# Kernel optimization log

Measured on AMD Instinct MI355X. Metric: run time of the kernel, lower is better.

Reference implementation:

```python
import jax, jax.numpy as jnp
import numpy as np

BS, LS, LL = 8, 64, 256          # batch, target len, source len
PS, D, NL, NH = 16000, 512, 4, 8 # vocab, d_model, n_layer, n_heads
DH = D // NH
DF = 4 * D


def _layer_norm(x, g, b, eps=1e-5):
    m = jnp.mean(x, -1, keepdims=True)
    v = jnp.var(x, -1, keepdims=True)
    return (x - m) * jax.lax.rsqrt(v + eps) * g + b


def setup_inputs() -> dict:
    key = jax.random.key(0)
    ks = jax.random.split(key, 20)
    s = 0.02
    return {
        "attn": jax.random.uniform(ks[0], (BS, LS, LL), jnp.float32),
        "mask": jnp.ones((BS, LL), dtype=bool),
        "tgt": jax.random.randint(ks[1], (BS, LS), 0, PS),
        "emb_w": jax.random.normal(ks[2], (PS, D), jnp.float32) * s,
        "Wq": jax.random.normal(ks[3], (NL, D, D), jnp.float32) * s,
        "Wk": jax.random.normal(ks[4], (NL, D, D), jnp.float32) * s,
        "Wv": jax.random.normal(ks[5], (NL, D, D), jnp.float32) * s,
        "Wo": jax.random.normal(ks[6], (NL, D, D), jnp.float32) * s,
        "ln1_g": jnp.ones((NL, D), jnp.float32),
        "ln1_b": jnp.zeros((NL, D), jnp.float32),
        "W1": jax.random.normal(ks[7], (NL, D, DF), jnp.float32) * s,
        "b1": jnp.zeros((NL, DF), jnp.float32),
        "W2": jax.random.normal(ks[8], (NL, DF, D), jnp.float32) * s,
        "b2": jnp.zeros((NL, D), jnp.float32),
        "ln2_g": jnp.ones((NL, D), jnp.float32),
        "ln2_b": jnp.zeros((NL, D), jnp.float32),
        "proj_w": jax.random.normal(ks[9], (PS, D), jnp.float32) * s,
    }


def reference(attn, mask, tgt, emb_w, Wq, Wk, Wv, Wo, ln1_g, ln1_b,
              W1, b1, W2, b2, ln2_g, ln2_b, proj_w):
    bs, ls = tgt.shape
    ll = attn.shape[2]
    ps = emb_w.shape[0]

    # --- scatter-add attention rows into vocab-aligned matrix (index_put_ accumulate=True) ---
    idx = (jnp.arange(bs)[:, None] * ps + tgt).reshape(-1)          # (bs*ls,)
    alg = jax.ops.segment_sum(attn.reshape(-1, ll), idx,
                              num_segments=bs * ps)                 # (bs*ps, ll)
    alg = alg.reshape(bs, ps, ll).transpose(0, 2, 1)                # (bs, ll, ps)
    alg = alg.at[:, :, 0].set(0.0)                                  # index_fill_ vocab id 0

    # --- transformer encoder over source positions ---
    x = alg @ emb_w                                                 # (bs, ll, D)
    pos = jnp.arange(ll, dtype=jnp.float32)[:, None]
    div = jnp.exp(jnp.arange(0, D, 2, dtype=jnp.float32) * (-np.log(10000.0) / D))
    pe = jnp.zeros((ll, D), jnp.float32)
    pe = pe.at[:, 0::2].set(jnp.sin(pos * div)).at[:, 1::2].set(jnp.cos(pos * div))
    x = x * np.sqrt(D).astype(np.float32) + pe

    bias = jnp.where(mask[:, None, None, :], 0.0, -1e9).astype(x.dtype)  # (bs,1,1,ll)
    scale = 1.0 / np.sqrt(DH).astype(np.float32)
    for i in range(Wq.shape[0]):
        q = (x @ Wq[i]).reshape(bs, ll, NH, DH)
        k = (x @ Wk[i]).reshape(bs, ll, NH, DH)
        v = (x @ Wv[i]).reshape(bs, ll, NH, DH)
        s = jnp.einsum('bqhd,bkhd->bhqk', q, k) * scale + bias
        a = jax.nn.softmax(s, axis=-1)
        o = jnp.einsum('bhqk,bkhd->bqhd', a, v).reshape(bs, ll, D) @ Wo[i]
        x = _layer_norm(x + o, ln1_g[i], ln1_b[i])
        f = jax.nn.relu(x @ W1[i] + b1[i]) @ W2[i] + b2[i]
        x = _layer_norm(x + f, ln2_g[i], ln2_b[i])

    return x @ proj_w.T                                             # (bs, ll, ps)
```

## Files before the change

kernel.cpp:

```cpp
#include <hip/hip_runtime.h>
#include <hip/hip_bf16.h>

#define BS 8
#define LS 64
#define LL 256
#define PS 16000
#define D  512
#define NL 4
#define NH 8
#define DH 64
#define DF 2048
#define ROWS (BS*LL)

typedef __attribute__((ext_vector_type(8))) __bf16 bf16x8;
typedef __attribute__((ext_vector_type(4))) float f32x4;
typedef __hip_bfloat16 hbf16;

static __device__ inline unsigned short f2bfu(float f) {
  hbf16 h = __float2bfloat16(f);
  return *reinterpret_cast<unsigned short*>(&h);
}

#define GLL16(g, l) __builtin_amdgcn_global_load_lds( \
    (const __attribute__((address_space(1))) unsigned int*)(g), \
    (__attribute__((address_space(3))) unsigned int*)(l), 16, 0, 0)

__global__ __launch_bounds__(256) void init_kernel(
    const float* __restrict__ Wq, const float* __restrict__ Wk,
    const float* __restrict__ Wv, const float* __restrict__ Wo,
    const float* __restrict__ W1, const float* __restrict__ W2,
    const float* __restrict__ proj,
    const float* __restrict__ attn, const int* __restrict__ tgt,
    const float* __restrict__ emb,
    hbf16* __restrict__ qkvT, hbf16* __restrict__ woT,
    hbf16* __restrict__ w1T, hbf16* __restrict__ w2T,
    hbf16* __restrict__ projT, hbf16* __restrict__ xb) {
  int id = blockIdx.x;
  if (id >= 14288) {
    int bl = id - 14288;
    int b = bl >> 8, l = bl & 255;
    int d0 = threadIdx.x;
    const float* ap = attn + (size_t)(b*LS)*LL + l;
    const int* tp = tgt + b*LS;
    float acc0 = 0.f, acc1 = 0.f;
    for (int s = 0; s < LS; ++s) {
      int t = tp[s];
      if (t != 0) {
        float a = ap[s*LL];
        acc0 = fmaf(a, emb[(size_t)t*D + d0],        acc0);
        acc1 = fmaf(a, emb[(size_t)t*D + d0 + 256],  acc1);
      }
    }
    const float sq = 22.62741699796952f;
    const float c  = -9.210340371976184f / 512.0f;
    {
      int d = d0;
      float freq = expf((float)(2*(d >> 1)) * c);
      float ang = (float)l * freq;
      float pe = (d & 1) ? cosf(ang) : sinf(ang);
      xb[(size_t)bl*D + d] = __float2bfloat16(acc0 * sq + pe);
    }
    {
      int d = d0 + 256;
      float freq = expf((float)(2*(d >> 1)) * c);
      float ang = (float)l * freq;
      float pe = (d & 1) ? cosf(ang) : sinf(ang);
      xb[(size_t)bl*D + d] = __float2bfloat16(acc1 * sq + pe);
    }
    return;
  }
  if (id >= 12288) {
    int i = (id - 12288) * 4096 + threadIdx.x * 4;
#pragma unroll
    for (int q = 0; q < 4; ++q) {
      int j = i + q*1024;
      float4 w = *(const float4*)(proj + j);
      ushort4 o;
      o.x = f2bfu(w.x); o.y = f2bfu(w.y); o.z = f2bfu(w.z); o.w = f2bfu(w.w);
      *(ushort4*)(projT + j) = o;
    }
    return;
  }
  const float* src; hbf16* dst; int R, C, r0, c0;
  if (id < 3072) {
    int zz = id >> 8, t = id & 255;
    int layer = zz / 3, which = zz % 3;
    src = (which == 0 ? Wq : which == 1 ? Wk : Wv) + (size_t)layer*D*D;
    dst = qkvT + (size_t)layer*3*D*D + (size_t)which*D*D;
    R = D; C = D; r0 = (t >> 4)*32; c0 = (t & 15)*32;
  } else if (id < 4096) {
    int t = id - 3072; int zz = t >> 8; t &= 255;
    src = Wo + (size_t)zz*D*D; dst = woT + (size_t)zz*D*D;
    R = D; C = D; r0 = (t >> 4)*32; c0 = (t & 15)*32;
  } else if (id < 8192) {
    int t = id - 4096; int zz = t >> 10; t &= 1023;
    src = W1 + (size_t)zz*D*DF; dst = w1T + (size_t)zz*D*DF;
    R = D; C = DF; r0 = (t >> 6)*32; c0 = (t & 63)*32;
  } else {
    int t = id - 8192; int zz = t >> 10; t &= 1023;
    src = W2 + (size_t)zz*DF*D; dst = w2T + (size_t)zz*DF*D;
    R = DF; C = D; r0 = (t >> 4)*32; c0 = (t & 15)*32;
  }
  __shared__ float tls[32][33];
  int tx = threadIdx.x & 31, ty = threadIdx.x >> 5;
#pragma unroll
  for (int i = 0; i < 4; ++i)
    tls[ty + i*8][tx] = src[(size_t)(r0 + ty + i*8)*C + c0 + tx];
  __syncthreads();
#pragma unroll
  for (int i = 0; i < 4; ++i)
    dst[(size_t)(c0 + ty + i*8)*R + r0 + tx] = __float2bfloat16(tls[tx][ty + i*8]);
}

template<int MF, int OUTMODE, int HASBIAS, int RELU, int BMODE, int SWZ>
__global__ __launch_bounds__(512) void mgemm(
    const __bf16* __restrict__ A, const __bf16* __restrict__ B,
    const float* __restrict__ bias, void* __restrict__ C0,
    __bf16* __restrict__ vt, int N, int K, int lda, int ldb, int ldc) {
  constexpr int TM = MF * 64;
  constexpr int NA = MF / 2;
  __shared__ __bf16 As[3][TM*32];
  __shared__ __bf16 Bs[3][128*32];
  const int z = blockIdx.z;
  if (BMODE == 3) {
    A += (size_t)z*K;
    B += (size_t)z*K;
    C0 = (void*)((char*)C0 + (size_t)z*ROWS*ldc*(OUTMODE == 0 ? 4 : 2));
  }
  int bm, bn;
  if (SWZ) {
    int nwg = gridDim.x * gridDim.y;
    int flat = blockIdx.y * gridDim.x + blockIdx.x;
    int swz = (flat & 7) * (nwg >> 3) + (flat >> 3);
    bm = swz % gridDim.x; bn = swz / gridDim.x;
  } else { bm = blockIdx.y; bn = blockIdx.x; }
  int tid = threadIdx.x;
  int wave = tid >> 6, lane = tid & 63;
  int m0 = bm * TM, n0 = bn * 128;
  int sr = lane >> 2;
  int sc = ((lane & 3) ^ ((lane >> 3) & 3)) * 8;
  const __bf16* ap = A + (size_t)(m0 + wave*16*NA + sr)*lda + sc;
  const __bf16* bp = B + (size_t)(n0 + wave*16 + sr)*ldb + sc;
  int wr = wave >> 1, wc = wave & 1;
  int lr = lane & 15, kg = lane >> 4;
  f32x4 acc[MF][4];
#pragma unroll
  for (int m = 0; m < MF; ++m)
#pragma unroll
    for (int n = 0; n < 4; ++n)
      acc[m][n] = (f32x4){0.f, 0.f, 0.f, 0.f};

  auto STAGE = [&](int buf, int k0) {
#pragma unroll
    for (int j = 0; j < NA; ++j)
      GLL16(ap + (size_t)(j*16)*lda + k0, &As[buf][(wave*16*NA + j*16)*32]);
    GLL16(bp + k0, &Bs[buf][(wave*16)*32]);
  };

  STAGE(0, 0);
  if (K > 32) STAGE(1, 32);
  int cur = 0;
  for (int k0 = 0; k0 < K; k0 += 32) {
    if (k0 + 32 < K) {
      if (NA == 1) asm volatile("s_waitcnt vmcnt(2)" ::: "memory");
      else         asm volatile("s_waitcnt vmcnt(3)" ::: "memory");
    } else         asm volatile("s_waitcnt vmcnt(0)" ::: "memory");
    __builtin_amdgcn_s_barrier();
    if (k0 + 64 < K) {
      int nxt = cur + 2; if (nxt >= 3) nxt -= 3;
      STAGE(nxt, k0 + 64);
    }
    bf16x8 af[MF], bfr[4];
#pragma unroll
    for (int m = 0; m < MF; ++m) {
      int rA = wr*(MF*16) + m*16 + lr;
      af[m] = *(const bf16x8*)&As[cur][rA*32 + ((kg ^ ((rA >> 1) & 3))*8)];
    }
#pragma unroll
    for (int n = 0; n < 4; ++n) {
      int rB = wc*64 + n*16 + lr;
      bfr[n] = *(const bf16x8*)&Bs[cur][rB*32 + ((kg ^ ((rB >> 1) & 3))*8)];
    }
#pragma unroll
    for (int m = 0; m < MF; ++m)
#pragma unroll
      for (int n = 0; n < 4; ++n)
        acc[m][n] = __builtin_amdgcn_mfma_f32_16x16x32_bf16(af[m], bfr[n], acc[m][n], 0, 0, 0);
    cur = (cur == 2) ? 0 : cur + 1;
  }
#pragma unroll
  for (int m = 0; m < MF; ++m) {
#pragma unroll
    for (int n = 0; n < 4; ++n) {
      int cc = n0 + wc*64 + n*16 + lr;
      float bv = 0.f;
      if (HASBIAS) bv = (BMODE != 3 || z == 0) ? bias[cc] : 0.f;
#pragma unroll
      for (int r = 0; r < 4; ++r) {
        int rr = m0 + wr*(MF*16) + m*16 + kg*4 + r;
        float v = acc[m][n][r] + bv;
        if (RELU) v = fmaxf(v, 0.f);
        if (OUTMODE == 0)      ((float*)C0)[(size_t)rr*ldc + cc] = v;
        else if (OUTMODE == 1) ((__bf16*)C0)[(size_t)rr*ldc + cc] = (__bf16)v;
        else {
          if (cc < 1024) ((__bf16*)C0)[(size_t)rr*ldc + cc] = (__bf16)v;
          else {
            int dd = cc - 1024; int h = dd >> 6; int d2 = dd & 63;
            int b = rr >> 8; int l = rr & 255;
            vt[((size_t)(b*8 + h)*DH + d2)*LL + l] = (__bf16)v;
          }
        }
      }
    }
  }
}

__global__ __launch_bounds__(256) void fattn_kernel(
    const __bf16* __restrict__ qkv,
    const __bf16* __restrict__ vt,
    __bf16* __restrict__ o) {
  __shared__ __bf16 Qs[64*64];
  __shared__ __bf16 Ks[256*64];
  __shared__ __bf16 Vs[64*256];
  int blk = blockIdx.x;
  int qc = blk & 3, h = (blk >> 2) & 7, b = blk >> 5;
  int tid = threadIdx.x, wave = tid >> 6, lane = tid & 63;
  const int rowbase = b*LL, q0 = qc*64;
  {
    int r8 = lane >> 3, c = lane & 7;
#pragma unroll
    for (int t = 0; t < 2; ++t) {
      int r = wave*16 + t*8 + r8;
      uint4 v = *(const uint4*)(qkv + (size_t)(rowbase + q0 + r)*1536 + h*64 + c*8);
      *(uint4*)&Qs[r*64 + ((c ^ (r & 7))*8)] = v;
    }
#pragma unroll
    for (int t = 0; t < 8; ++t) {
      int r = wave*64 + t*8 + r8;
      uint4 v = *(const uint4*)(qkv + (size_t)(rowbase + r)*1536 + 512 + h*64 + c*8);
      *(uint4*)&Ks[r*64 + ((c ^ (r & 7))*8)] = v;
    }
    const __bf16* vb = vt + (size_t)(b*8 + h)*DH*LL;
    int d2 = lane >> 5, c32 = lane & 31;
#pragma unroll
    for (int t = 0; t < 8; ++t) {
      int d = wave*16 + t*2 + d2;
      uint4 v = *(const uint4*)(vb + (size_t)d*LL + c32*8);
      *(uint4*)&Vs[d*256 + ((c32 ^ (d & 7))*8)] = v;
    }
  }
  __syncthreads();
  int lr = lane & 15, kg = lane >> 4;
  f32x4 sacc[16];
#pragma unroll
  for (int n = 0; n < 16; ++n) sacc[n] = (f32x4){0.f,0.f,0.f,0.f};
#pragma unroll
  for (int j = 0; j < 2; ++j) {
    int ck = j*4 + kg;
    int rq = wave*16 + lr;
    bf16x8 af = *(const bf16x8*)&Qs[rq*64 + ((ck ^ (rq & 7))*8)];
#pragma unroll
    for (int n = 0; n < 16; ++n) {
      int rk = n*16 + lr;
      bf16x8 bk = *(const bf16x8*)&Ks[rk*64 + ((ck ^ (rk & 7))*8)];
      sacc[n] = __builtin_amdgcn_mfma_f32_16x16x32_bf16(af, bk, sacc[n], 0, 0, 0);
    }
  }
  __syncthreads();
  __bf16* Ps = &Ks[wave*16*256];
#pragma unroll
  for (int r = 0; r < 4; ++r) {
    float mx = -1e30f;
#pragma unroll
    for (int n = 0; n < 16; ++n) mx = fmaxf(mx, sacc[n][r]);
#pragma unroll
    for (int off = 8; off >= 1; off >>= 1) mx = fmaxf(mx, __shfl_xor(mx, off, 64));
    mx *= 0.125f;
    float sum = 0.f;
    float pv[16];
#pragma unroll
    for (int n = 0; n < 16; ++n) {
      pv[n] = __expf(sacc[n][r]*0.125f - mx);
      sum += pv[n];
    }
#pragma unroll
    for (int off = 8; off >= 1; off >>= 1) sum += __shfl_xor(sum, off, 64);
    float inv = 1.0f / sum;
    int row = kg*4 + r;
#pragma unroll
    for (int n = 0; n < 16; ++n) {
      int col = n*16 + lr;
      int cc = col >> 3;
      Ps[row*256 + ((cc ^ (row & 7))*8) + (col & 7)] = (__bf16)(pv[n]*inv);
    }
  }
  f32x4 oacc[4];
#pragma unroll
  for (int n = 0; n < 4; ++n) oacc[n] = (f32x4){0.f,0.f,0.f,0.f};
#pragma unroll
  for (int kk = 0; kk < 8; ++kk) {
    int ck = kk*4 + kg;
    bf16x8 pa = *(const bf16x8*)&Ps[lr*256 + ((ck ^ (lr & 7))*8)];
#pragma unroll
    for (int n = 0; n < 4; ++n) {
      int dv = n*16 + lr;
      bf16x8 bv = *(const bf16x8*)&Vs[dv*256 + ((ck ^ (dv & 7))*8)];
      oacc[n] = __builtin_amdgcn_mfma_f32_16x16x32_bf16(pa, bv, oacc[n], 0, 0, 0);
    }
  }
#pragma unroll
  for (int n = 0; n < 4; ++n)
#pragma unroll
    for (int r = 0; r < 4; ++r) {
      int row = rowbase + q0 + wave*16 + kg*4 + r;
      int col = h*64 + n*16 + lr;
      o[(size_t)row*D + col] = (__bf16)oacc[n][r];
    }
}

template<int NS>
__global__ __launch_bounds__(256) void ln_kernel(
    hbf16* __restrict__ xb, const __bf16* __restrict__ delta,
    const float* __restrict__ g, const float* __restrict__ bb) {
  int row = blockIdx.x*4 + (threadIdx.x >> 6);
  int lane = threadIdx.x & 63;
  size_t base = (size_t)row*D + lane*8;
  bf16x8 xv = *(const bf16x8*)((const __bf16*)xb + base);
  float h[8];
#pragma unroll
  for (int i = 0; i < 8; ++i) h[i] = (float)xv[i];
#pragma unroll
  for (int p = 0; p < NS; ++p) {
    bf16x8 dv = *(const bf16x8*)(delta + (size_t)p*ROWS*D + base);
#pragma unroll
    for (int i = 0; i < 8; ++i) h[i] += (float)dv[i];
  }
  float s = 0.f, s2 = 0.f;
#pragma unroll
  for (int i = 0; i < 8; ++i) { s += h[i]; s2 += h[i]*h[i]; }
#pragma unroll
  for (int off = 32; off >= 1; off >>= 1) {
    s  += __shfl_xor(s,  off, 64);
    s2 += __shfl_xor(s2, off, 64);
  }
  float mean = s * (1.f/512.f);
  float var  = s2 * (1.f/512.f) - mean*mean;
  float rs = rsqrtf(var + 1e-5f);
  int c = lane*8;
  bf16x8 ov;
#pragma unroll
  for (int i = 0; i < 8; ++i)
    ov[i] = (__bf16)((h[i] - mean) * rs * g[c+i] + bb[c+i]);
  *(bf16x8*)((__bf16*)xb + base) = ov;
}

extern "C" void kernel_launch(void* const* d_in, const int* in_sizes, int n_in,
                              void* d_out, int out_size, void* d_ws, size_t ws_size,
                              hipStream_t stream) {
  const float* attn = (const float*)d_in[0];
  const int*   tgt  = (const int*)d_in[2];
  const float* emb  = (const float*)d_in[3];
  const float* Wq   = (const float*)d_in[4];
  const float* Wk   = (const float*)d_in[5];
  const float* Wv   = (const float*)d_in[6];
  const float* Wo   = (const float*)d_in[7];
  const float* ln1g = (const float*)d_in[8];
  const float* ln1b = (const float*)d_in[9];
  const float* W1   = (const float*)d_in[10];
  const float* b1   = (const float*)d_in[11];
  const float* W2   = (const float*)d_in[12];
  const float* b2   = (const float*)d_in[13];
  const float* ln2g = (const float*)d_in[14];
  const float* ln2b = (const float*)d_in[15];
  const float* proj = (const float*)d_in[16];
  float* out = (float*)d_out;

  char* p = (char*)d_ws;
  auto alloc = [&](size_t bytes) { char* r = p; p += bytes; return (void*)r; };
  hbf16* tb   = (hbf16*)alloc((size_t)4*ROWS*D*2);
  hbf16* xb   = (hbf16*)alloc((size_t)ROWS*D*2);
  hbf16* ob   = (hbf16*)alloc((size_t)ROWS*D*2);
  hbf16* vt   = (hbf16*)alloc((size_t)BS*NH*DH*LL*2);
  char*  R0   = (char*)alloc((size_t)ROWS*DF*2);
  hbf16* wqkvT= (hbf16*)alloc((size_t)NL*3*D*D*2);
  hbf16* woT  = (hbf16*)alloc((size_t)NL*D*D*2);
  hbf16* w1T  = (hbf16*)alloc((size_t)NL*D*DF*2);
  hbf16* w2T  = (hbf16*)alloc((size_t)NL*DF*D*2);
  hbf16* projT= (hbf16*)alloc((size_t)PS*D*2);
  hbf16* qkvb = (hbf16*)R0;
  hbf16* hb   = (hbf16*)R0;

  init_kernel<<<12288 + PS*D/4096 + ROWS, 256, 0, stream>>>(
      Wq, Wk, Wv, Wo, W1, W2, proj, attn, tgt, emb,
      wqkvT, woT, w1T, w2T, projT, xb);

  for (int i = 0; i < NL; ++i) {
    mgemm<2,3,0,0,0,0><<<dim3(12,16,1), 512, 0, stream>>>(
        (const __bf16*)xb, (const __bf16*)(wqkvT + (size_t)i*3*D*D),
        nullptr, qkvb, (__bf16*)vt, 3*D, D, D, D, 3*D);
    fattn_kernel<<<BS*NH*4, 256, 0, stream>>>(
        (const __bf16*)qkvb, (const __bf16*)vt, (__bf16*)ob);
    mgemm<2,1,0,0,3,0><<<dim3(4,16,4), 512, 0, stream>>>(
        (const __bf16*)ob, (const __bf16*)(woT + (size_t)i*D*D),
        nullptr, tb, nullptr, D, 128, D, D, D);
    ln_kernel<4><<<ROWS/4, 256, 0, stream>>>(xb, (const __bf16*)tb,
                                             ln1g + i*D, ln1b + i*D);
    mgemm<2,1,1,1,0,0><<<dim3(16,16,1), 512, 0, stream>>>(
        (const __bf16*)xb, (const __bf16*)(w1T + (size_t)i*D*DF),
        b1 + (size_t)i*DF, hb, nullptr, DF, D, D, D, DF);
    mgemm<2,1,1,0,3,0><<<dim3(4,16,4), 512, 0, stream>>>(
        (const __bf16*)hb, (const __bf16*)(w2T + (size_t)i*DF*D),
        b2 + (size_t)i*D, tb, nullptr, D, 512, DF, DF, D);
    ln_kernel<4><<<ROWS/4, 256, 0, stream>>>(xb, (const __bf16*)tb,
                                             ln2g + i*D, ln2b + i*D);
  }

  mgemm<4,0,0,0,0,1><<<dim3(8,125,1), 512, 0, stream>>>(
      (const __bf16*)xb, (const __bf16*)projT, nullptr, out, nullptr,
      PS, D, D, D, PS);
}
```

Baseline: 353.3 us.

## Fuse residual LayerNorm into split-K GEMM epilogue via atomic row-block barrier

Removes the separate LayerNorm kernels. The Wo and W2 split-K GEMMs now wait on a per-row-block atomic counter until all 16 tiles for that row block are written, then each block normalizes its share of rows (residual plus four partial sums) and writes back to xb. This saves two kernel launches per layer and one round of reading the partials. The cost is a spin-wait inter-block barrier, which relies on all 256 blocks being co-resident and on cumulative counter targets across layers.

Measured after the change: 1.249 ms. 3.54x slower.

```diff
diff --git a/kernel.cpp b/kernel.cpp
--- a/kernel.cpp
+++ b/kernel.cpp
@@ -34,8 +34,10 @@
     const float* __restrict__ emb,
     hbf16* __restrict__ qkvT, hbf16* __restrict__ woT,
     hbf16* __restrict__ w1T, hbf16* __restrict__ w2T,
-    hbf16* __restrict__ projT, hbf16* __restrict__ xb) {
+    hbf16* __restrict__ projT, hbf16* __restrict__ xb,
+    int* __restrict__ cnt) {
   int id = blockIdx.x;
+  if (id == 0 && threadIdx.x < 16) cnt[threadIdx.x] = 0;
   if (id >= 14288) {
     int bl = id - 14288;
     int b = bl >> 8, l = bl & 255;
@@ -112,16 +114,18 @@
     dst[(size_t)(c0 + ty + i*8)*R + r0 + tx] = __float2bfloat16(tls[tx][ty + i*8]);
 }
 
-template<int MF, int OUTMODE, int HASBIAS, int RELU, int BMODE, int SWZ>
+template<int MF, int OUTMODE, int HASBIAS, int RELU, int BMODE, int SWZ, int LNF>
 __global__ __launch_bounds__(512) void mgemm(
     const __bf16* __restrict__ A, const __bf16* __restrict__ B,
-    const float* __restrict__ bias, void* __restrict__ C0,
-    __bf16* __restrict__ vt, int N, int K, int lda, int ldb, int ldc) {
+    const float* __restrict__ bias, void* C0,
+    __bf16* __restrict__ vt, int N, int K, int lda, int ldb, int ldc,
+    const float* lng, const float* lnb, hbf16* xb, int* cnt, int ctarget) {
   constexpr int TM = MF * 64;
   constexpr int NA = MF / 2;
   __shared__ __bf16 As[3][TM*32];
   __shared__ __bf16 Bs[3][128*32];
   const int z = blockIdx.z;
+  __bf16* tb0 = (__bf16*)C0;
   if (BMODE == 3) {
     A += (size_t)z*K;
     B += (size_t)z*K;
@@ -213,6 +217,46 @@
       }
     }
   }
+  if (LNF) {
+    __threadfence();
+    __syncthreads();
+    if (tid == 0) {
+      atomicAdd(&cnt[bm], 1);
+      while (atomicAdd(&cnt[bm], 0) < ctarget) __builtin_amdgcn_s_sleep(8);
+    }
+    __syncthreads();
+    __threadfence();
+    int slot = z*4 + bn;
+    int r = bm*128 + slot*8 + wave;
+    size_t base = (size_t)r*D + lane*8;
+    bf16x8 xv = *(const bf16x8*)((const __bf16*)xb + base);
+    float h[8];
+#pragma unroll
+    for (int i = 0; i < 8; ++i) h[i] = (float)xv[i];
+#pragma unroll
+    for (int p = 0; p < 4; ++p) {
+      bf16x8 dv = *(const bf16x8*)(tb0 + (size_t)p*ROWS*ldc + base);
+#pragma unroll
+      for (int i = 0; i < 8; ++i) h[i] += (float)dv[i];
+    }
+    float s = 0.f, s2 = 0.f;
+#pragma unroll
+    for (int i = 0; i < 8; ++i) { s += h[i]; s2 += h[i]*h[i]; }
+#pragma unroll
+    for (int off = 32; off >= 1; off >>= 1) {
+      s  += __shfl_xor(s,  off, 64);
+      s2 += __shfl_xor(s2, off, 64);
+    }
+    float mean = s * (1.f/512.f);
+    float var  = s2 * (1.f/512.f) - mean*mean;
+    float rs = rsqrtf(var + 1e-5f);
+    int c = lane*8;
+    bf16x8 ov;
+#pragma unroll
+    for (int i = 0; i < 8; ++i)
+      ov[i] = (__bf16)((h[i] - mean) * rs * lng[c+i] + lnb[c+i]);
+    *(bf16x8*)((__bf16*)xb + base) = ov;
+  }
 }
 
 __global__ __launch_bounds__(256) void fattn_kernel(
@@ -316,42 +360,6 @@
       int col = h*64 + n*16 + lr;
       o[(size_t)row*D + col] = (__bf16)oacc[n][r];
     }
-}
-
-template<int NS>
-__global__ __launch_bounds__(256) void ln_kernel(
-    hbf16* __restrict__ xb, const __bf16* __restrict__ delta,
-    const float* __restrict__ g, const float* __restrict__ bb) {
-  int row = blockIdx.x*4 + (threadIdx.x >> 6);
-  int lane = threadIdx.x & 63;
-  size_t base = (size_t)row*D + lane*8;
-  bf16x8 xv = *(const bf16x8*)((const __bf16*)xb + base);
-  float h[8];
-#pragma unroll
-  for (int i = 0; i < 8; ++i) h[i] = (float)xv[i];
-#pragma unroll
-  for (int p = 0; p < NS; ++p) {
-    bf16x8 dv = *(const bf16x8*)(delta + (size_t)p*ROWS*D + base);
-#pragma unroll
-    for (int i = 0; i < 8; ++i) h[i] += (float)dv[i];
-  }
-  float s = 0.f, s2 = 0.f;
-#pragma unroll
-  for (int i = 0; i < 8; ++i) { s += h[i]; s2 += h[i]*h[i]; }
-#pragma unroll
-  for (int off = 32; off >= 1; off >>= 1) {
-    s  += __shfl_xor(s,  off, 64);
-    s2 += __shfl_xor(s2, off, 64);
-  }
-  float mean = s * (1.f/512.f);
-  float var  = s2 * (1.f/512.f) - mean*mean;
-  float rs = rsqrtf(var + 1e-5f);
-  int c = lane*8;
-  bf16x8 ov;
-#pragma unroll
-  for (int i = 0; i < 8; ++i)
-    ov[i] = (__bf16)((h[i] - mean) * rs * g[c+i] + bb[c+i]);
-  *(bf16x8*)((__bf16*)xb + base) = ov;
 }
 
 extern "C" void kernel_launch(void* const* d_in, const int* in_sizes, int n_in,
@@ -387,35 +395,36 @@
   hbf16* w1T  = (hbf16*)alloc((size_t)NL*D*DF*2);
   hbf16* w2T  = (hbf16*)alloc((size_t)NL*DF*D*2);
   hbf16* projT= (hbf16*)alloc((size_t)PS*D*2);
+  int*   cnt  = (int*)alloc(64*sizeof(int));
   hbf16* qkvb = (hbf16*)R0;
   hbf16* hb   = (hbf16*)R0;
 
   init_kernel<<<12288 + PS*D/4096 + ROWS, 256, 0, stream>>>(
       Wq, Wk, Wv, Wo, W1, W2, proj, attn, tgt, emb,
-      wqkvT, woT, w1T, w2T, projT, xb);
+      wqkvT, woT, w1T, w2T, projT, xb, cnt);
 
   for (int i = 0; i < NL; ++i) {
-    mgemm<2,3,0,0,0,0><<<dim3(12,16,1), 512, 0, stream>>>(
+    mgemm<2,3,0,0,0,0,0><<<dim3(12,16,1), 512, 0, stream>>>(
         (const __bf16*)xb, (const __bf16*)(wqkvT + (size_t)i*3*D*D),
-        nullptr, qkvb, (__bf16*)vt, 3*D, D, D, D, 3*D);
+        nullptr, qkvb, (__bf16*)vt, 3*D, D, D, D, 3*D,
+        nullptr, nullptr, nullptr, nullptr, 0);
     fattn_kernel<<<BS*NH*4, 256, 0, stream>>>(
         (const __bf16*)qkvb, (const __bf16*)vt, (__bf16*)ob);
-    mgemm<2,1,0,0,3,0><<<dim3(4,16,4), 512, 0, stream>>>(
+    mgemm<2,1,0,0,3,0,1><<<dim3(4,16,4), 512, 0, stream>>>(
         (const __bf16*)ob, (const __bf16*)(woT + (size_t)i*D*D),
-        nullptr, tb, nullptr, D, 128, D, D, D);
-    ln_kernel<4><<<ROWS/4, 256, 0, stream>>>(xb, (const __bf16*)tb,
-                                             ln1g + i*D, ln1b + i*D);
-    mgemm<2,1,1,1,0,0><<<dim3(16,16,1), 512, 0, stream>>>(
+        nullptr, tb, nullptr, D, 128, D, D, D,
+        ln1g + i*D, ln1b + i*D, xb, cnt, 16*(2*i+1));
+    mgemm<2,1,1,1,0,0,0><<<dim3(16,16,1), 512, 0, stream>>>(
         (const __bf16*)xb, (const __bf16*)(w1T + (size_t)i*D*DF),
-        b1 + (size_t)i*DF, hb, nullptr, DF, D, D, D, DF);
-    mgemm<2,1,1,0,3,0><<<dim3(4,16,4), 512, 0, stream>>>(
+        b1 + (size_t)i*DF, hb, nullptr, DF, D, D, D, DF,
+        nullptr, nullptr, nullptr, nullptr, 0);
+    mgemm<2,1,1,0,3,0,1><<<dim3(4,16,4), 512, 0, stream>>>(
         (const __bf16*)hb, (const __bf16*)(w2T + (size_t)i*DF*D),
-        b2 + (size_t)i*D, tb, nullptr, D, 512, DF, DF, D);
-    ln_kernel<4><<<ROWS/4, 256, 0, stream>>>(xb, (const __bf16*)tb,
-                                             ln2g + i*D, ln2b + i*D);
-  }
-
-  mgemm<4,0,0,0,0,1><<<dim3(8,125,1), 512, 0, stream>>>(
+        b2 + (size_t)i*D, tb, nullptr, D, 512, DF, DF, D,
+        ln2g + i*D, ln2b + i*D, xb, cnt, 16*(2*i+2));
+  }
+
+  mgemm<4,0,0,0,0,1,0><<<dim3(8,125,1), 512, 0, stream>>>(
       (const __bf16*)xb, (const __bf16*)projT, nullptr, out, nullptr,
-      PS, D, D, D, PS);
+      PS, D, D, D, PS, nullptr, nullptr, nullptr, nullptr, 0);
 }
```
